# Kernel optimization log

Measured on AMD Instinct MI355X. Metric: run time of the kernel, lower is better.

The kernel has to match this reference:

```python
import math
import jax, jax.numpy as jnp
import numpy as np

BATCH = 2048
LATENT = 64
BETA = 6.0
LOG_2PI = math.log(2.0 * math.pi)


def setup_inputs() -> dict:
    key = jax.random.key(0)
    k1, k2, k3 = jax.random.split(key, 3)
    z = jax.random.normal(k1, (BATCH, LATENT), dtype=jnp.float32)
    z_mean = jax.random.normal(k2, (BATCH, LATENT), dtype=jnp.float32)
    z_logvar = jax.random.normal(k3, (BATCH, LATENT), dtype=jnp.float32)
    return {"z": z, "z_mean": z_mean, "z_logvar": z_logvar}


def _gaussian_log_density(samples, mean, log_var):
    # elementwise Gaussian log-density, broadcasts to [B, B, L]
    inv_sigma = jnp.exp(-log_var)
    tmp = samples - mean
    return -0.5 * (tmp * tmp * inv_sigma + log_var + LOG_2PI)


def _total_correlation(z, z_mean, z_logvar):
    # log q(z_i | x_j) per-dim: [B, B, L]
    log_qz_prob = _gaussian_log_density(z[:, None, :], z_mean[None, :, :], z_logvar[None, :, :])
    # log prod_l (1/B) sum_j q(z_l | x_j)  (constants dropped as in original)
    log_qz_product = jnp.sum(jax.scipy.special.logsumexp(log_qz_prob, axis=1), axis=1)  # [B]
    # log (1/B) sum_j q(z | x_j)
    log_qz = jax.scipy.special.logsumexp(jnp.sum(log_qz_prob, axis=2), axis=1)  # [B]
    return jnp.mean(log_qz - log_qz_product)


def _gaussian_kl(z_mean, z_logvar):
    # standard KL(q(z|x) || N(0, I)), mean over batch
    return 0.5 * jnp.mean(
        jnp.sum(jnp.square(z_mean) + jnp.exp(z_logvar) - z_logvar - 1.0, axis=1)
    )


def reference(z, z_mean, z_logvar):
    kl_loss = _gaussian_kl(z_mean, z_logvar)
    tc = (BETA - 1.0) * _total_correlation(z, z_mean, z_logvar)
    return tc + kl_loss
```

## Files before the change

kernel.cpp:

```cpp
#include <hip/hip_runtime.h>
#include <hip/hip_bf16.h>
#include <math.h>

#define BATCH 2048
#define LATENT 64
#define LOG_2PI 1.8378770664093453f
#define BETA_M1 5.0f
#define LN2 0.69314718055994530942f
#define C2 (-0.72134752044448170368f)

#define OFF_VT   0
#define OFF_TCE  (128*BATCH)
#define OFF_UP   (OFF_TCE + 64*BATCH)
#define OFF_CE   (OFF_UP + 128*BATCH)
#define OFF_KLP  (OFF_CE + BATCH)
#define OFF_RMP  (OFF_KLP + BATCH)
#define OFF_RSP  (OFF_RMP + 2*BATCH)
#define OFF_PART (OFF_RSP + 2*BATCH)
#define OFF_PP   (OFF_PART + 16)

__global__ __launch_bounds__(256) void precompute_kernel(const float* __restrict__ z,
                                                         const float* __restrict__ zm,
                                                         const float* __restrict__ zlv,
                                                         float* __restrict__ ws) {
    __shared__ float Tz[64][65], Tm[64][65], Tlv[64][65];
    __shared__ float CEp[4][64], KLp[4][64];
    int t = threadIdx.x, lane = t & 63, w = t >> 6;
    int j0 = blockIdx.x * 64;

    #pragma unroll
    for (int p = 0; p < 16; ++p) {
        int jr = p * 4 + w;
        int idx = (j0 + jr) * LATENT + lane;
        Tz[jr][lane]  = z[idx];
        Tm[jr][lane]  = zm[idx];
        Tlv[jr][lane] = zlv[idx];
    }
    __syncthreads();

    int j = j0 + lane;
    float ce_acc = 0.0f, kl_acc = 0.0f;
    #pragma unroll
    for (int q = 0; q < 16; ++q) {
        int l = q * 4 + w;
        float zv = Tz[lane][l];
        float m  = Tm[lane][l];
        float lv = Tlv[lane][l];
        float iv  = __expf(-lv);
        float civ = C2 * iv;
        float miv = m * iv;
        float cmv = C2 * miv;
        float cev = C2 * fmaf(m, miv, lv + LOG_2PI);
        ws[OFF_VT  + (2*l)   * BATCH + j] = civ;
        ws[OFF_VT  + (2*l+1) * BATCH + j] = cmv;
        ws[OFF_TCE + l       * BATCH + j] = cev;
        ws[OFF_UP  + (2*l)   * BATCH + j] = zv * zv;
        ws[OFF_UP  + (2*l+1) * BATCH + j] = -2.0f * zv;
        ce_acc += cev;
        kl_acc += fmaf(m, m, __expf(lv)) - lv - 1.0f;
    }
    CEp[w][lane] = ce_acc;
    KLp[w][lane] = kl_acc;
    __syncthreads();
    if (w == 0) {
        ws[OFF_CE  + j] = CEp[0][lane] + CEp[1][lane] + CEp[2][lane] + CEp[3][lane];
        ws[OFF_KLP + j] = KLp[0][lane] + KLp[1][lane] + KLp[2][lane] + KLp[3][lane];
    }
}

#define DIMB 1024
#define ROWB 512
__global__ __launch_bounds__(256) void main_kernel(float* __restrict__ ws) {
    __shared__ float RMs[8][4], RSs[8][4];
    int bx = blockIdx.x, t = threadIdx.x;

    if (bx < DIMB) {
        int l  = bx >> 4;
        int ic = (bx >> 3) & 1;
        int jc = bx & 7;
        int ib = ic * 1024 + t;

        const float* __restrict__ up0 = ws + OFF_UP + (2*l)   * BATCH;
        const float* __restrict__ up1 = ws + OFF_UP + (2*l+1) * BATCH;
        float z2_0 = up0[ib],       z2_1 = up0[ib + 256],
              z2_2 = up0[ib + 512], z2_3 = up0[ib + 768];
        float n2_0 = up1[ib],       n2_1 = up1[ib + 256],
              n2_2 = up1[ib + 512], n2_3 = up1[ib + 768];

        const float* __restrict__ pc = ws + OFF_VT  + (2*l)   * BATCH + jc * 256;
        const float* __restrict__ pm = ws + OFF_VT  + (2*l+1) * BATCH + jc * 256;
        const float* __restrict__ pe = ws + OFF_TCE + l       * BATCH + jc * 256;

        float s0 = 0.f, s1 = 0.f, s2 = 0.f, s3 = 0.f;
        for (int jj = 0; jj < 256; jj += 8) {
            #pragma unroll
            for (int u = 0; u < 8; ++u) {
                float cc = pc[jj + u];
                float mm = pm[jj + u];
                float ee = pe[jj + u];
                s0 += __builtin_amdgcn_exp2f(fmaf(z2_0, cc, fmaf(n2_0, mm, ee)));
                s1 += __builtin_amdgcn_exp2f(fmaf(z2_1, cc, fmaf(n2_1, mm, ee)));
                s2 += __builtin_amdgcn_exp2f(fmaf(z2_2, cc, fmaf(n2_2, mm, ee)));
                s3 += __builtin_amdgcn_exp2f(fmaf(z2_3, cc, fmaf(n2_3, mm, ee)));
            }
        }
        __hip_bfloat16* pp = (__hip_bfloat16*)(ws + OFF_PP);
        size_t base = ((size_t)(jc * 64 + l)) * BATCH;
        pp[base + ib]       = __float2bfloat16(s0);
        pp[base + ib + 256] = __float2bfloat16(s1);
        pp[base + ib + 512] = __float2bfloat16(s2);
        pp[base + ib + 768] = __float2bfloat16(s3);
    } else {
        int bx2 = bx - DIMB;
        int ib8 = bx2 >> 1, ph = bx2 & 1;
        int i0 = ib8 * 8;
        int jb = ph * 1024 + 4 * t;
        int lane = t & 63, w = t >> 6;

        const float* __restrict__ Vt = ws + OFF_VT;
        const float* __restrict__ Up = ws + OFF_UP;

        float r[8][4];
        #pragma unroll
        for (int i = 0; i < 8; ++i)
            r[i][0] = r[i][1] = r[i][2] = r[i][3] = 0.0f;

        for (int l = 0; l < LATENT; ++l) {
            float4 v0 = *(const float4*)(Vt + (2*l)   * BATCH + jb);
            float4 v1 = *(const float4*)(Vt + (2*l+1) * BATCH + jb);
            const float* __restrict__ u0 = Up + (2*l)   * BATCH + i0;
            const float* __restrict__ u1 = Up + (2*l+1) * BATCH + i0;
            #pragma unroll
            for (int i = 0; i < 8; ++i) {
                float a = u0[i], b = u1[i];
                r[i][0] = fmaf(a, v0.x, fmaf(b, v1.x, r[i][0]));
                r[i][1] = fmaf(a, v0.y, fmaf(b, v1.y, r[i][1]));
                r[i][2] = fmaf(a, v0.z, fmaf(b, v1.z, r[i][2]));
                r[i][3] = fmaf(a, v0.w, fmaf(b, v1.w, r[i][3]));
            }
        }

        float4 ce4 = *(const float4*)(ws + OFF_CE + jb);
        #pragma unroll
        for (int i = 0; i < 8; ++i) {
            float rc0 = r[i][0] + ce4.x, rc1 = r[i][1] + ce4.y;
            float rc2 = r[i][2] + ce4.z, rc3 = r[i][3] + ce4.w;
            float M = fmaxf(fmaxf(rc0, rc1), fmaxf(rc2, rc3));
            float S = __builtin_amdgcn_exp2f(rc0 - M) + __builtin_amdgcn_exp2f(rc1 - M)
                    + __builtin_amdgcn_exp2f(rc2 - M) + __builtin_amdgcn_exp2f(rc3 - M);
            #pragma unroll
            for (int off = 32; off > 0; off >>= 1) {
                float Mo = __shfl_xor(M, off, 64);
                float So = __shfl_xor(S, off, 64);
                float mn = fmaxf(M, Mo);
                S = S * __builtin_amdgcn_exp2f(M - mn) + So * __builtin_amdgcn_exp2f(Mo - mn);
                M = mn;
            }
            if (lane == 0) { RMs[i][w] = M; RSs[i][w] = S; }
        }
        __syncthreads();
        if (t < 8) {
            float M = RMs[t][0], S = RSs[t][0];
            #pragma unroll
            for (int w2 = 1; w2 < 4; ++w2) {
                float Mo = RMs[t][w2], So = RSs[t][w2];
                float mn = fmaxf(M, Mo);
                S = S * __builtin_amdgcn_exp2f(M - mn) + So * __builtin_amdgcn_exp2f(Mo - mn);
                M = mn;
            }
            ws[OFF_RMP + ph * BATCH + i0 + t] = M;
            ws[OFF_RSP + ph * BATCH + i0 + t] = S;
        }
    }
}

__global__ __launch_bounds__(256) void finalize1_kernel(const float* __restrict__ ws,
                                                        float* __restrict__ wso) {
    __shared__ float s_tc[256];
    __shared__ float s_kl[256];
    int t = threadIdx.x;
    int i = blockIdx.x * 256 + t;

    const __hip_bfloat16* __restrict__ pp = (const __hip_bfloat16*)(ws + OFF_PP);
    float sp = 0.0f;
    for (int l = 0; l < LATENT; ++l) {
        float s = 0.0f;
        #pragma unroll
        for (int c = 0; c < 8; ++c)
            s += __bfloat162float(pp[((size_t)(c * 64 + l)) * BATCH + i]);
        sp += __builtin_amdgcn_logf(s);
    }

    float M0 = ws[OFF_RMP + i], M1 = ws[OFF_RMP + BATCH + i];
    float S0 = ws[OFF_RSP + i], S1 = ws[OFF_RSP + BATCH + i];
    float mn = fmaxf(M0, M1);
    float lqz = mn + __builtin_amdgcn_logf(
        S0 * __builtin_amdgcn_exp2f(M0 - mn) + S1 * __builtin_amdgcn_exp2f(M1 - mn));

    s_tc[t] = lqz - sp;
    s_kl[t] = ws[OFF_KLP + i];
    __syncthreads();
    for (int s = 128; s > 0; s >>= 1) {
        if (t < s) { s_tc[t] += s_tc[t + s]; s_kl[t] += s_kl[t + s]; }
        __syncthreads();
    }
    if (t == 0) {
        wso[OFF_PART + blockIdx.x]     = s_tc[0];
        wso[OFF_PART + 8 + blockIdx.x] = s_kl[0];
    }
}

__global__ void finalize2_kernel(const float* __restrict__ ws,
                                 float* __restrict__ out) {
    if (threadIdx.x == 0) {
        float tc = 0.0f, kl = 0.0f;
        #pragma unroll
        for (int b = 0; b < 8; ++b) {
            tc += ws[OFF_PART + b];
            kl += ws[OFF_PART + 8 + b];
        }
        out[0] = BETA_M1 * (LN2 * tc / (float)BATCH) + 0.5f * (kl / (float)BATCH);
    }
}

extern "C" void kernel_launch(void* const* d_in, const int* in_sizes, int n_in,
                              void* d_out, int out_size, void* d_ws, size_t ws_size,
                              hipStream_t stream) {
    const float* z        = (const float*)d_in[0];
    const float* z_mean   = (const float*)d_in[1];
    const float* z_logvar = (const float*)d_in[2];
    float* out = (float*)d_out;
    float* ws  = (float*)d_ws;

    precompute_kernel<<<32, 256, 0, stream>>>(z, z_mean, z_logvar, ws);
    main_kernel<<<DIMB + ROWB, 256, 0, stream>>>(ws);
    finalize1_kernel<<<8, 256, 0, stream>>>(ws, ws);
    finalize2_kernel<<<1, 64, 0, stream>>>(ws, out);
}
```

Before: 128.6 us.

## Widen precompute and finalize grids, give each dim-block eight rows

The precompute kernel now runs 128 blocks of 16 rows instead of 32 blocks of 64, so more CUs share the setup work. The finalize stage moves from 8 blocks that each loop over all 64 latent dims to 128 blocks that split the (l, i) logs across threads, combined with atomicAdd into a buffer zeroed by precompute. The per-dimension logsumexp blocks of main_kernel each handle 8 rows per thread instead of 4, which halves their count and reuses each loaded column value more. The risks are lower occupancy from extra registers in main_kernel, fewer blocks to balance against the row blocks, and a float atomic sum whose order is not deterministic.

Result: faster. 119.2 us (-7.4%).

```diff
diff --git a/kernel.cpp b/kernel.cpp
--- a/kernel.cpp
+++ b/kernel.cpp
@@ -23,29 +23,31 @@
                                                          const float* __restrict__ zm,
                                                          const float* __restrict__ zlv,
                                                          float* __restrict__ ws) {
-    __shared__ float Tz[64][65], Tm[64][65], Tlv[64][65];
-    __shared__ float CEp[4][64], KLp[4][64];
+    __shared__ float Tz[16][65], Tm[16][65], Tlv[16][65];
+    __shared__ float CEp[16][16], KLp[16][16];
     int t = threadIdx.x, lane = t & 63, w = t >> 6;
-    int j0 = blockIdx.x * 64;
+    int j0 = blockIdx.x * 16;
 
     #pragma unroll
-    for (int p = 0; p < 16; ++p) {
+    for (int p = 0; p < 4; ++p) {
         int jr = p * 4 + w;
         int idx = (j0 + jr) * LATENT + lane;
         Tz[jr][lane]  = z[idx];
         Tm[jr][lane]  = zm[idx];
         Tlv[jr][lane] = zlv[idx];
     }
+    if (blockIdx.x == 0 && t < 16) ws[OFF_PART + t] = 0.0f;
     __syncthreads();
 
-    int j = j0 + lane;
+    int jl = t & 15, lg = t >> 4;
+    int j = j0 + jl;
     float ce_acc = 0.0f, kl_acc = 0.0f;
     #pragma unroll
-    for (int q = 0; q < 16; ++q) {
-        int l = q * 4 + w;
-        float zv = Tz[lane][l];
-        float m  = Tm[lane][l];
-        float lv = Tlv[lane][l];
+    for (int q = 0; q < 4; ++q) {
+        int l = q * 16 + lg;
+        float zv = Tz[jl][l];
+        float m  = Tm[jl][l];
+        float lv = Tlv[jl][l];
         float iv  = __expf(-lv);
         float civ = C2 * iv;
         float miv = m * iv;
@@ -59,57 +61,62 @@
         ce_acc += cev;
         kl_acc += fmaf(m, m, __expf(lv)) - lv - 1.0f;
     }
-    CEp[w][lane] = ce_acc;
-    KLp[w][lane] = kl_acc;
+    CEp[lg][jl] = ce_acc;
+    KLp[lg][jl] = kl_acc;
     __syncthreads();
-    if (w == 0) {
-        ws[OFF_CE  + j] = CEp[0][lane] + CEp[1][lane] + CEp[2][lane] + CEp[3][lane];
-        ws[OFF_KLP + j] = KLp[0][lane] + KLp[1][lane] + KLp[2][lane] + KLp[3][lane];
-    }
-}
-
-#define DIMB 1024
+    if (t < 16) {
+        float ce = 0.0f, kl = 0.0f;
+        #pragma unroll
+        for (int g = 0; g < 16; ++g) { ce += CEp[g][t]; kl += KLp[g][t]; }
+        ws[OFF_CE  + j0 + t] = ce;
+        ws[OFF_KLP + j0 + t] = kl;
+    }
+}
+
+#define DIMB 512
 #define ROWB 512
 __global__ __launch_bounds__(256) void main_kernel(float* __restrict__ ws) {
     __shared__ float RMs[8][4], RSs[8][4];
     int bx = blockIdx.x, t = threadIdx.x;
 
     if (bx < DIMB) {
-        int l  = bx >> 4;
-        int ic = (bx >> 3) & 1;
+        int l  = bx >> 3;
         int jc = bx & 7;
-        int ib = ic * 1024 + t;
 
         const float* __restrict__ up0 = ws + OFF_UP + (2*l)   * BATCH;
         const float* __restrict__ up1 = ws + OFF_UP + (2*l+1) * BATCH;
-        float z2_0 = up0[ib],       z2_1 = up0[ib + 256],
-              z2_2 = up0[ib + 512], z2_3 = up0[ib + 768];
-        float n2_0 = up1[ib],       n2_1 = up1[ib + 256],
-              n2_2 = up1[ib + 512], n2_3 = up1[ib + 768];
+        float z2[8], n2[8];
+        #pragma unroll
+        for (int k = 0; k < 8; ++k) {
+            z2[k] = up0[t + 256*k];
+            n2[k] = up1[t + 256*k];
+        }
 
         const float* __restrict__ pc = ws + OFF_VT  + (2*l)   * BATCH + jc * 256;
         const float* __restrict__ pm = ws + OFF_VT  + (2*l+1) * BATCH + jc * 256;
         const float* __restrict__ pe = ws + OFF_TCE + l       * BATCH + jc * 256;
 
-        float s0 = 0.f, s1 = 0.f, s2 = 0.f, s3 = 0.f;
+        float s[8];
+        #pragma unroll
+        for (int k = 0; k < 8; ++k) s[k] = 0.0f;
+
         for (int jj = 0; jj < 256; jj += 8) {
             #pragma unroll
             for (int u = 0; u < 8; ++u) {
                 float cc = pc[jj + u];
                 float mm = pm[jj + u];
                 float ee = pe[jj + u];
-                s0 += __builtin_amdgcn_exp2f(fmaf(z2_0, cc, fmaf(n2_0, mm, ee)));
-                s1 += __builtin_amdgcn_exp2f(fmaf(z2_1, cc, fmaf(n2_1, mm, ee)));
-                s2 += __builtin_amdgcn_exp2f(fmaf(z2_2, cc, fmaf(n2_2, mm, ee)));
-                s3 += __builtin_amdgcn_exp2f(fmaf(z2_3, cc, fmaf(n2_3, mm, ee)));
-            }
-        }
+                #pragma unroll
+                for (int k = 0; k < 8; ++k)
+                    s[k] += __builtin_amdgcn_exp2f(fmaf(z2[k], cc, fmaf(n2[k], mm, ee)));
+            }
+        }
+
         __hip_bfloat16* pp = (__hip_bfloat16*)(ws + OFF_PP);
         size_t base = ((size_t)(jc * 64 + l)) * BATCH;
-        pp[base + ib]       = __float2bfloat16(s0);
-        pp[base + ib + 256] = __float2bfloat16(s1);
-        pp[base + ib + 512] = __float2bfloat16(s2);
-        pp[base + ib + 768] = __float2bfloat16(s3);
+        #pragma unroll
+        for (int k = 0; k < 8; ++k)
+            pp[base + t + 256*k] = __float2bfloat16(s[k]);
     } else {
         int bx2 = bx - DIMB;
         int ib8 = bx2 >> 1, ph = bx2 & 1;
@@ -174,51 +181,53 @@
     }
 }
 
-__global__ __launch_bounds__(256) void finalize1_kernel(const float* __restrict__ ws,
-                                                        float* __restrict__ wso) {
+__global__ __launch_bounds__(256) void finalize_kernel(float* __restrict__ ws) {
     __shared__ float s_tc[256];
     __shared__ float s_kl[256];
     int t = threadIdx.x;
-    int i = blockIdx.x * 256 + t;
+    int gid = blockIdx.x * 256 + t;
 
     const __hip_bfloat16* __restrict__ pp = (const __hip_bfloat16*)(ws + OFF_PP);
-    float sp = 0.0f;
-    for (int l = 0; l < LATENT; ++l) {
+
+    float acc = 0.0f, kl = 0.0f;
+    #pragma unroll
+    for (int k = 0; k < 4; ++k) {
+        int f = gid + 32768 * k;
+        int l = f >> 11, i = f & 2047;
         float s = 0.0f;
         #pragma unroll
         for (int c = 0; c < 8; ++c)
             s += __bfloat162float(pp[((size_t)(c * 64 + l)) * BATCH + i]);
-        sp += __builtin_amdgcn_logf(s);
-    }
-
-    float M0 = ws[OFF_RMP + i], M1 = ws[OFF_RMP + BATCH + i];
-    float S0 = ws[OFF_RSP + i], S1 = ws[OFF_RSP + BATCH + i];
-    float mn = fmaxf(M0, M1);
-    float lqz = mn + __builtin_amdgcn_logf(
-        S0 * __builtin_amdgcn_exp2f(M0 - mn) + S1 * __builtin_amdgcn_exp2f(M1 - mn));
-
-    s_tc[t] = lqz - sp;
-    s_kl[t] = ws[OFF_KLP + i];
+        acc -= __builtin_amdgcn_logf(s);
+    }
+
+    if (gid < BATCH) {
+        int i = gid;
+        float M0 = ws[OFF_RMP + i], M1 = ws[OFF_RMP + BATCH + i];
+        float S0 = ws[OFF_RSP + i], S1 = ws[OFF_RSP + BATCH + i];
+        float mn = fmaxf(M0, M1);
+        acc += mn + __builtin_amdgcn_logf(
+            S0 * __builtin_amdgcn_exp2f(M0 - mn) + S1 * __builtin_amdgcn_exp2f(M1 - mn));
+        kl = ws[OFF_KLP + i];
+    }
+
+    s_tc[t] = acc; s_kl[t] = kl;
     __syncthreads();
     for (int s = 128; s > 0; s >>= 1) {
         if (t < s) { s_tc[t] += s_tc[t + s]; s_kl[t] += s_kl[t + s]; }
         __syncthreads();
     }
     if (t == 0) {
-        wso[OFF_PART + blockIdx.x]     = s_tc[0];
-        wso[OFF_PART + 8 + blockIdx.x] = s_kl[0];
-    }
-}
-
-__global__ void finalize2_kernel(const float* __restrict__ ws,
-                                 float* __restrict__ out) {
+        atomicAdd(&ws[OFF_PART + 0], s_tc[0]);
+        atomicAdd(&ws[OFF_PART + 1], s_kl[0]);
+    }
+}
+
+__global__ void assemble_kernel(const float* __restrict__ ws,
+                                float* __restrict__ out) {
     if (threadIdx.x == 0) {
-        float tc = 0.0f, kl = 0.0f;
-        #pragma unroll
-        for (int b = 0; b < 8; ++b) {
-            tc += ws[OFF_PART + b];
-            kl += ws[OFF_PART + 8 + b];
-        }
+        float tc = ws[OFF_PART + 0];
+        float kl = ws[OFF_PART + 1];
         out[0] = BETA_M1 * (LN2 * tc / (float)BATCH) + 0.5f * (kl / (float)BATCH);
     }
 }
@@ -232,8 +241,8 @@
     float* out = (float*)d_out;
     float* ws  = (float*)d_ws;
 
-    precompute_kernel<<<32, 256, 0, stream>>>(z, z_mean, z_logvar, ws);
+    precompute_kernel<<<128, 256, 0, stream>>>(z, z_mean, z_logvar, ws);
     main_kernel<<<DIMB + ROWB, 256, 0, stream>>>(ws);
-    finalize1_kernel<<<8, 256, 0, stream>>>(ws, ws);
-    finalize2_kernel<<<1, 64, 0, stream>>>(ws, out);
-}
+    finalize_kernel<<<128, 256, 0, stream>>>(ws);
+    assemble_kernel<<<1, 64, 0, stream>>>(ws, out);
+}
```
